# Kernel tuning notes

Hardware: AMD Instinct MI355X
Metric: run time of the kernel (lower is better)

## Reference

```python
import jax, jax.numpy as jnp
import numpy as np

B, H, W, DIM, NH, WS, SS = 32, 56, 56, 512, 16, 7, 3
L = H * W
HD = DIM // NH
N = WS * WS
SCALE = HD ** -0.5
EPS = 1e-5


def _rel_pos_index():
    coords = np.stack(np.meshgrid(np.arange(WS), np.arange(WS), indexing='ij'))  # (2,ws,ws)
    cf = coords.reshape(2, -1)
    rc = (cf[:, :, None] - cf[:, None, :]).transpose(1, 2, 0).astype(np.int64)  # (N,N,2)
    rc[..., 0] += WS - 1
    rc[..., 1] += WS - 1
    rc[..., 0] *= 2 * WS - 1
    return rc.sum(-1)  # (N,N)


def _shift_mask():
    img = np.zeros((H, W), np.float32)
    cnt = 0
    for hs in (slice(0, -WS), slice(-WS, -SS), slice(-SS, None)):
        for ws_ in (slice(0, -WS), slice(-WS, -SS), slice(-SS, None)):
            img[hs, ws_] = cnt
            cnt += 1
    m = img.reshape(H // WS, WS, W // WS, WS).transpose(0, 2, 1, 3).reshape(-1, N)  # (nW,N)
    diff = m[:, None, :] - m[:, :, None]
    return np.where(diff != 0, -100.0, 0.0).astype(np.float32)  # (nW,N,N)


REL_IDX = jnp.asarray(_rel_pos_index())
ATTN_MASK = jnp.asarray(_shift_mask())


def _ln(x, g, b):
    mu = jnp.mean(x, -1, keepdims=True)
    var = jnp.var(x, -1, keepdims=True)
    return (x - mu) * jax.lax.rsqrt(var + EPS) * g + b


def setup_inputs() -> dict:
    key = jax.random.key(0)
    ks = jax.random.split(key, 8)
    s = 0.02
    return {
        'x': jax.random.normal(ks[0], (B, L, DIM), jnp.float32),
        'norm1_g': jnp.ones((DIM,), jnp.float32),
        'norm1_b': jnp.zeros((DIM,), jnp.float32),
        'qkv_w': jax.random.normal(ks[1], (DIM, 3 * DIM), jnp.float32) * s,
        'qkv_b': jnp.zeros((3 * DIM,), jnp.float32),
        'rel_bias_table': jax.random.normal(ks[2], ((2 * WS - 1) ** 2, NH), jnp.float32) * s,
        'proj_w': jax.random.normal(ks[3], (DIM, DIM), jnp.float32) * s,
        'proj_b': jnp.zeros((DIM,), jnp.float32),
        'norm2_g': jnp.ones((DIM,), jnp.float32),
        'norm2_b': jnp.zeros((DIM,), jnp.float32),
        'fc1_w': jax.random.normal(ks[4], (DIM, 4 * DIM), jnp.float32) * s,
        'fc1_b': jnp.zeros((4 * DIM,), jnp.float32),
        'fc2_w': jax.random.normal(ks[5], (4 * DIM, DIM), jnp.float32) * s,
        'fc2_b': jnp.zeros((DIM,), jnp.float32),
    }


def reference(x, norm1_g, norm1_b, qkv_w, qkv_b, rel_bias_table, proj_w, proj_b,
              norm2_g, norm2_b, fc1_w, fc1_b, fc2_w, fc2_b):
    shortcut = x
    h = _ln(x, norm1_g, norm1_b).reshape(B, H, W, DIM)
    # cyclic shift
    h = jnp.roll(h, (-SS, -SS), axis=(1, 2))
    # window partition -> (B*nW, N, C)
    nWh, nWw = H // WS, W // WS
    h = h.reshape(B, nWh, WS, nWw, WS, DIM).transpose(0, 1, 3, 2, 4, 5).reshape(-1, N, DIM)
    Bw = h.shape[0]
    # qkv
    qkv = (h @ qkv_w + qkv_b).reshape(Bw, N, 3, NH, HD).transpose(2, 0, 3, 1, 4)
    q, k, v = qkv[0], qkv[1], qkv[2]  # (Bw, NH, N, HD)
    attn = jnp.einsum('bhnd,bhmd->bhnm', q * SCALE, k)
    # relative position bias (NH, N, N)
    bias = rel_bias_table[REL_IDX.reshape(-1)].reshape(N, N, NH).transpose(2, 0, 1)
    attn = attn + bias[None]
    # shift mask: (B, nW, NH, N, N) + (1, nW, 1, N, N)
    nW = nWh * nWw
    attn = attn.reshape(B, nW, NH, N, N) + ATTN_MASK[None, :, None]
    attn = jax.nn.softmax(attn.reshape(Bw, NH, N, N), axis=-1)
    out = jnp.einsum('bhnm,bhmd->bhnd', attn, v).transpose(0, 2, 1, 3).reshape(Bw, N, DIM)
    out = out @ proj_w + proj_b
    # window reverse + reverse shift
    out = out.reshape(B, nWh, nWw, WS, WS, DIM).transpose(0, 1, 3, 2, 4, 5).reshape(B, H, W, DIM)
    out = jnp.roll(out, (SS, SS), axis=(1, 2)).reshape(B, L, DIM)
    x = shortcut + out
    # MLP (GELU exact, matching torch nn.GELU default)
    y = _ln(x, norm2_g, norm2_b)
    y = jax.nn.gelu(y @ fc1_w + fc1_b, approximate=False) @ fc2_w + fc2_b
    return x + y
```

## Files before the change

kernel.cpp:

```cpp
#include <hip/hip_runtime.h>
#include <hip/hip_bf16.h>
#include <math.h>

#define MROWS 100352
#define MHALF 50176
#define DIM   512
#define LL    3136
#define HH    56
#define SSH   3
#define SCALE_QK 0.17677669529663687f

typedef __bf16 bf16;
typedef __bf16 bf16x8 __attribute__((ext_vector_type(8)));
typedef float  f32x4  __attribute__((ext_vector_type(4)));

typedef __attribute__((address_space(1))) void* gas_ptr;
typedef __attribute__((address_space(3))) void* las_ptr;

__device__ __forceinline__ void gload_lds16(const void* g, void* l) {
  __builtin_amdgcn_global_load_lds((gas_ptr)g, (las_ptr)l, 16, 0, 0);
}

__device__ __forceinline__ int nat_row(int r) {
  int bw = r / 49;
  int n  = r - bw * 49;
  int b  = bw >> 6;
  int wh = (bw >> 3) & 7;
  int ww = bw & 7;
  int i  = n / 7;
  int j  = n - i * 7;
  int hs = wh * 7 + i + SSH; if (hs >= HH) hs -= HH;
  int ws = ww * 7 + j + SSH; if (ws >= HH) ws -= HH;
  return b * LL + hs * HH + ws;
}

__global__ __launch_bounds__(256) void tcast_kernel(const float* __restrict__ src,
                                                    bf16* __restrict__ dst,
                                                    int Kd, int Nd) {
  __shared__ float t[32][33];
  int tx = threadIdx.x & 31, ty = threadIdx.x >> 5;
  int n0 = blockIdx.x * 32, k0 = blockIdx.y * 32;
  #pragma unroll
  for (int yy = ty; yy < 32; yy += 8)
    t[yy][tx] = src[(size_t)(k0 + yy) * Nd + n0 + tx];
  __syncthreads();
  #pragma unroll
  for (int yy = ty; yy < 32; yy += 8)
    dst[(size_t)(n0 + yy) * Kd + k0 + tx] = (bf16)t[tx][yy];
}

template<int PERM>
__global__ __launch_bounds__(256) void ln_kernel(const float* __restrict__ x,
                                                 const float* __restrict__ gw,
                                                 const float* __restrict__ bw_,
                                                 bf16* __restrict__ out) {
  int wave = threadIdx.x >> 6, lane = threadIdx.x & 63;
  int r = blockIdx.x * 4 + wave;
  int src = PERM ? nat_row(r) : r;
  const float* px = x + (size_t)src * DIM + lane * 8;
  float4 v0 = *(const float4*)px;
  float4 v1 = *(const float4*)(px + 4);
  float s = v0.x + v0.y + v0.z + v0.w + v1.x + v1.y + v1.z + v1.w;
  float q = v0.x*v0.x + v0.y*v0.y + v0.z*v0.z + v0.w*v0.w
          + v1.x*v1.x + v1.y*v1.y + v1.z*v1.z + v1.w*v1.w;
  #pragma unroll
  for (int m = 1; m < 64; m <<= 1) { s += __shfl_xor(s, m); q += __shfl_xor(q, m); }
  float mean = s * (1.f / DIM);
  float var  = q * (1.f / DIM) - mean * mean;
  float rstd = rsqrtf(var + 1e-5f);
  int c0 = lane * 8;
  float4 g0 = *(const float4*)(gw + c0),  g1 = *(const float4*)(gw + c0 + 4);
  float4 b0 = *(const float4*)(bw_ + c0), b1 = *(const float4*)(bw_ + c0 + 4);
  bf16x8 o;
  o[0] = (bf16)((v0.x - mean) * rstd * g0.x + b0.x);
  o[1] = (bf16)((v0.y - mean) * rstd * g0.y + b0.y);
  o[2] = (bf16)((v0.z - mean) * rstd * g0.z + b0.z);
  o[3] = (bf16)((v0.w - mean) * rstd * g0.w + b0.w);
  o[4] = (bf16)((v1.x - mean) * rstd * g1.x + b1.x);
  o[5] = (bf16)((v1.y - mean) * rstd * g1.y + b1.y);
  o[6] = (bf16)((v1.z - mean) * rstd * g1.z + b1.z);
  o[7] = (bf16)((v1.w - mean) * rstd * g1.w + b1.w);
  *(bf16x8*)(out + (size_t)r * DIM + c0) = o;
}


#define MF(a,b,c) __builtin_amdgcn_mfma_f32_16x16x32_bf16((a),(b),(c),0,0,0)
#define BAR() __builtin_amdgcn_s_barrier()
#define WLG() asm volatile("s_waitcnt lgkmcnt(0)" ::: "memory")
#define WVM(n) asm volatile("s_waitcnt vmcnt(" #n ")" ::: "memory")

template<int MODE, int KD, int ND>
__global__ __launch_bounds__(512, 2) void gemm256_kernel(const bf16* __restrict__ A,
                                                         const bf16* __restrict__ Bt,
                                                         const float* __restrict__ bias,
                                                         const float* __restrict__ resid,
                                                         bf16* __restrict__ outB,
                                                         float* __restrict__ outF) {
  constexpr int NTN = ND / 256;
  constexpr int NI  = KD / 128;
  __shared__ bf16 lds[65536];

  const int tid = threadIdx.x, lane = tid & 63, wv = tid >> 6;
  const int lr = lane & 15, lg = lane >> 4;
  const int wm = wv >> 2, wn = wv & 3;

  int nwg = gridDim.x, orig = blockIdx.x;
  int q = nwg >> 3, r = nwg & 7, xcd = orig & 7;
  int wgid = (xcd < r ? xcd * (q + 1) : r * (q + 1) + (xcd - r) * q) + (orig >> 3);
  int tm = wgid / NTN, tn = wgid % NTN;

  const bf16* gA = A  + (size_t)tm * 256 * KD;
  const bf16* gB = Bt + (size_t)tn * 256 * KD;

  const int klg  = (lg * 8) ^ ((lr & 8) ? 16 : 0);
  const int a_rd = (wm * 128 + lr) * 32 + klg;
  const int b_rd = (wn * 64 + lr) * 32 + klg;

  const int kbOffE = (wv >> 2) * 8192;
  const int kGlob  = (wv >> 2) * 32 + (((lane & 3) * 8) ^ ((lane & 32) ? 16 : 0));
  const int rl0    = ((wv * 2) & 7) * 16 + (lane >> 2);
  const int rl1    = rl0 + 16;
  const int c0off  = ((wv * 2) & 7) * 512;

#define STG(GP, DB, h, koff) \
  gload_lds16((GP) + (size_t)((h) * 128 + rl0) * KD + (koff) + kGlob, \
              (void*)(lds + (DB) + kbOffE + (h) * 4096 + c0off)); \
  gload_lds16((GP) + (size_t)((h) * 128 + rl1) * KD + (koff) + kGlob, \
              (void*)(lds + (DB) + kbOffE + (h) * 4096 + c0off + 512));

  f32x4 acc[8][4];
  #pragma unroll
  for (int i = 0; i < 8; i++)
    #pragma unroll
    for (int j = 0; j < 4; j++) { acc[i][j][0]=0.f; acc[i][j][1]=0.f; acc[i][j][2]=0.f; acc[i][j][3]=0.f; }

  bf16x8 Af[4][2], Bf0[2][2], Bf1[2][2];

  STG(gA, 0,     0, 0)  STG(gA, 0,     1, 0)
  STG(gB, 16384, 0, 0)  STG(gB, 16384, 1, 0)
  STG(gA, 32768, 0, 64) STG(gA, 32768, 1, 64)
  STG(gB, 49152, 0, 64) STG(gB, 49152, 1, 64)
  WVM(8); BAR();

#define PHASES(AB, BB, DOST, KST, ENDW) { \
     \
    _Pragma("unroll") for (int m = 0; m < 4; m++) { \
      Af[m][0] = *(const bf16x8*)(lds + (AB) + m * 512 + a_rd); \
      Af[m][1] = *(const bf16x8*)(lds + (AB) + 8192 + m * 512 + a_rd); } \
    _Pragma("unroll") for (int n = 0; n < 2; n++) { \
      Bf0[n][0] = *(const bf16x8*)(lds + (BB) + n * 512 + b_rd); \
      Bf0[n][1] = *(const bf16x8*)(lds + (BB) + 8192 + n * 512 + b_rd); } \
    BAR(); WLG(); __builtin_amdgcn_s_setprio(1); \
    _Pragma("unroll") for (int m = 0; m < 4; m++) \
      _Pragma("unroll") for (int n = 0; n < 2; n++) { \
        acc[m][n] = MF(Af[m][0], Bf0[n][0], acc[m][n]); \
        acc[m][n] = MF(Af[m][1], Bf0[n][1], acc[m][n]); } \
    __builtin_amdgcn_s_setprio(0); BAR(); \
     \
    _Pragma("unroll") for (int n = 0; n < 2; n++) { \
      Bf1[n][0] = *(const bf16x8*)(lds + (BB) + (n + 2) * 512 + b_rd); \
      Bf1[n][1] = *(const bf16x8*)(lds + (BB) + 8192 + (n + 2) * 512 + b_rd); } \
    if (DOST) { STG(gB, (BB), 0, (KST)) } \
    BAR(); WLG(); __builtin_amdgcn_s_setprio(1); \
    _Pragma("unroll") for (int m = 0; m < 4; m++) \
      _Pragma("unroll") for (int n = 0; n < 2; n++) { \
        acc[m][n + 2] = MF(Af[m][0], Bf1[n][0], acc[m][n + 2]); \
        acc[m][n + 2] = MF(Af[m][1], Bf1[n][1], acc[m][n + 2]); } \
    __builtin_amdgcn_s_setprio(0); BAR(); \
     \
    _Pragma("unroll") for (int m = 0; m < 4; m++) { \
      Af[m][0] = *(const bf16x8*)(lds + (AB) + (m + 4) * 512 + a_rd); \
      Af[m][1] = *(const bf16x8*)(lds + (AB) + 8192 + (m + 4) * 512 + a_rd); } \
    if (DOST) { STG(gB, (BB), 1, (KST)) STG(gA, (AB), 0, (KST)) } \
    BAR(); WLG(); __builtin_amdgcn_s_setprio(1); \
    _Pragma("unroll") for (int m = 0; m < 4; m++) \
      _Pragma("unroll") for (int n = 0; n < 2; n++) { \
        acc[m + 4][n + 2] = MF(Af[m][0], Bf1[n][0], acc[m + 4][n + 2]); \
        acc[m + 4][n + 2] = MF(Af[m][1], Bf1[n][1], acc[m + 4][n + 2]); } \
    __builtin_amdgcn_s_setprio(0); BAR(); \
     \
    if (DOST) { STG(gA, (AB), 1, (KST)) } \
    BAR(); WLG(); __builtin_amdgcn_s_setprio(1); \
    _Pragma("unroll") for (int m = 0; m < 4; m++) \
      _Pragma("unroll") for (int n = 0; n < 2; n++) { \
        acc[m + 4][n] = MF(Af[m][0], Bf0[n][0], acc[m + 4][n]); \
        acc[m + 4][n] = MF(Af[m][1], Bf0[n][1], acc[m + 4][n]); } \
    __builtin_amdgcn_s_setprio(0); ENDW; BAR(); \
  }

  #pragma unroll 1
  for (int I = 0; I < NI - 1; ++I) {
    int ke = (2 * I + 2) * 64;
    PHASES(0,     16384, 1, ke,      WVM(6));
    PHASES(32768, 49152, 1, ke + 64, WVM(6));
  }
  PHASES(0,     16384, 0, 0, WVM(0));
  PHASES(32768, 49152, 0, 0, ((void)0));

#undef PHASES
#undef STG

  #pragma unroll
  for (int fm = 0; fm < 8; fm++) {
    #pragma unroll
    for (int rr = 0; rr < 4; rr++) {
      int row = tm * 256 + wm * 128 + fm * 16 + lg * 4 + rr;
      int orow = (MODE == 1) ? nat_row(row) : row;
      #pragma unroll
      for (int fn = 0; fn < 4; fn++) {
        int col = tn * 256 + wn * 64 + fn * 16 + lr;
        float v = acc[fm][fn][rr] + bias[col];
        if (MODE == 0) {
          outB[(size_t)row * ND + col] = (bf16)v;
        } else if (MODE == 1) {
          outF[(size_t)orow * ND + col] = resid[(size_t)orow * ND + col] + v;
        } else if (MODE == 2) {
          float g = 0.5f * v * (1.f + erff(v * 0.70710678118654752f));
          outB[(size_t)row * ND + col] = (bf16)g;
        } else {
          outF[(size_t)row * ND + col] = resid[(size_t)row * ND + col] + v;
        }
      }
    }
  }
}

__global__ __launch_bounds__(256) void attn_kernel(const bf16* __restrict__ qkv,
                                                   const float* __restrict__ table,
                                                   bf16* __restrict__ attnO) {
  __shared__ bf16 P[4][64 * 72];
  int wave = threadIdx.x >> 6, lane = threadIdx.x & 63;
  int lr = lane & 15, lg = lane >> 4;
  int wid = blockIdx.x * 4 + wave;
  int win = wid >> 4, head = wid & 15;
  int wh = (win >> 3) & 7, ww = win & 7;
  const bf16* base = qkv + (size_t)win * (49 * 1536) + head * 32;

  f32x4 zero4 = {0.f, 0.f, 0.f, 0.f};
  bf16x8 aq[4], bk[4];
  #pragma unroll
  for (int mi = 0; mi < 4; mi++) {
    int qq = mi * 16 + lr; if (qq > 48) qq = 48;
    aq[mi] = *(const bf16x8*)(base + qq * 1536 + lg * 8);
    bk[mi] = *(const bf16x8*)(base + 512 + qq * 1536 + lg * 8);
  }
  f32x4 sacc[4][4];
  #pragma unroll
  for (int mi = 0; mi < 4; mi++)
    #pragma unroll
    for (int ni = 0; ni < 4; ni++)
      sacc[mi][ni] = __builtin_amdgcn_mfma_f32_16x16x32_bf16(aq[mi], bk[ni], zero4, 0, 0, 0);

  float rsum[4][4];
  #pragma unroll
  for (int mi = 0; mi < 4; mi++) {
    #pragma unroll
    for (int rr = 0; rr < 4; rr++) {
      int qrow = mi * 16 + lg * 4 + rr;
      int qc = qrow > 48 ? 48 : qrow;
      int i1 = qc / 7, j1 = qc - i1 * 7;
      int labq = ((wh < 7) ? 0 : ((i1 < 4) ? 1 : 2)) * 3 + ((ww < 7) ? 0 : ((j1 < 4) ? 1 : 2));
      float pv[4];
      float mv = -3.0e30f;
      #pragma unroll
      for (int ni = 0; ni < 4; ni++) {
        int key = ni * 16 + lr;
        float v;
        if (key > 48) {
          v = -1e30f;
        } else {
          int i2 = key / 7, j2 = key - i2 * 7;
          int labk = ((wh < 7) ? 0 : ((i2 < 4) ? 1 : 2)) * 3 + ((ww < 7) ? 0 : ((j2 < 4) ? 1 : 2));
          int idx = (i1 - i2 + 6) * 13 + (j1 - j2 + 6);
          float msk = (labq == labk) ? 0.f : -100.f;
          v = sacc[mi][ni][rr] * SCALE_QK + table[idx * 16 + head] + msk;
        }
        pv[ni] = v;
        mv = fmaxf(mv, v);
      }
      #pragma unroll
      for (int m = 1; m < 16; m <<= 1) mv = fmaxf(mv, __shfl_xor(mv, m));
      float sum = 0.f;
      #pragma unroll
      for (int ni = 0; ni < 4; ni++) {
        float p = __expf(pv[ni] - mv);
        sum += p;
        P[wave][qrow * 72 + ni * 16 + lr] = (bf16)p;
      }
      #pragma unroll
      for (int m = 1; m < 16; m <<= 1) sum += __shfl_xor(sum, m);
      rsum[mi][rr] = sum;
    }
  }
  __syncthreads();

  f32x4 oacc[4][2];
  #pragma unroll
  for (int mi = 0; mi < 4; mi++) { oacc[mi][0] = zero4; oacc[mi][1] = zero4; }
  #pragma unroll
  for (int ks = 0; ks < 2; ks++) {
    bf16x8 bv[2];
    #pragma unroll
    for (int n2 = 0; n2 < 2; n2++) {
      #pragma unroll
      for (int j = 0; j < 8; j++) {
        int kv = ks * 32 + lg * 8 + j; if (kv > 48) kv = 48;
        bv[n2][j] = base[1024 + (size_t)kv * 1536 + n2 * 16 + lr];
      }
    }
    #pragma unroll
    for (int mi = 0; mi < 4; mi++) {
      bf16x8 ap = *(const bf16x8*)(&P[wave][(mi * 16 + lr) * 72 + ks * 32 + lg * 8]);
      #pragma unroll
      for (int n2 = 0; n2 < 2; n2++)
        oacc[mi][n2] = __builtin_amdgcn_mfma_f32_16x16x32_bf16(ap, bv[n2], oacc[mi][n2], 0, 0, 0);
    }
  }
  #pragma unroll
  for (int mi = 0; mi < 4; mi++) {
    #pragma unroll
    for (int rr = 0; rr < 4; rr++) {
      int qrow = mi * 16 + lg * 4 + rr;
      if (qrow < 49) {
        float inv = 1.f / rsum[mi][rr];
        #pragma unroll
        for (int n2 = 0; n2 < 2; n2++)
          attnO[((size_t)win * 49 + qrow) * DIM + head * 32 + n2 * 16 + lr] =
              (bf16)(oacc[mi][n2][rr] * inv);
      }
    }
  }
}

extern "C" void kernel_launch(void* const* d_in, const int* in_sizes, int n_in,
                              void* d_out, int out_size, void* d_ws, size_t ws_size,
                              hipStream_t stream) {
  const float* x      = (const float*)d_in[0];
  const float* n1g    = (const float*)d_in[1];
  const float* n1b    = (const float*)d_in[2];
  const float* qkv_w  = (const float*)d_in[3];
  const float* qkv_b  = (const float*)d_in[4];
  const float* tabl   = (const float*)d_in[5];
  const float* proj_w = (const float*)d_in[6];
  const float* proj_b = (const float*)d_in[7];
  const float* n2g    = (const float*)d_in[8];
  const float* n2b    = (const float*)d_in[9];
  const float* fc1_w  = (const float*)d_in[10];
  const float* fc1_b  = (const float*)d_in[11];
  const float* fc2_w  = (const float*)d_in[12];
  const float* fc2_b  = (const float*)d_in[13];
  float* out = (float*)d_out;

  char* ws = (char*)d_ws;
  bf16*  RegA   = (bf16*)ws;
  bf16*  RegB   = (bf16*)(ws + 102760448);
  float* x2     = (float*)(ws + 102760448 + 308281344);
  bf16*  qkvWt  = (bf16*)(ws + 102760448 + 308281344 + 205520896);
  bf16*  projWt = qkvWt + 1536 * 512;
  bf16*  fc1Wt  = projWt + 512 * 512;
  bf16*  fc2Wt  = fc1Wt + 2048 * 512;

  tcast_kernel<<<dim3(1536 / 32, 512 / 32), 256, 0, stream>>>(qkv_w, qkvWt, 512, 1536);
  tcast_kernel<<<dim3(512 / 32, 512 / 32), 256, 0, stream>>>(proj_w, projWt, 512, 512);
  tcast_kernel<<<dim3(2048 / 32, 512 / 32), 256, 0, stream>>>(fc1_w, fc1Wt, 512, 2048);
  tcast_kernel<<<dim3(512 / 32, 2048 / 32), 256, 0, stream>>>(fc2_w, fc2Wt, 2048, 512);

  ln_kernel<1><<<MROWS / 4, 256, 0, stream>>>(x, n1g, n1b, RegA);
  gemm256_kernel<0, 512, 1536><<<(MROWS / 256) * 6, 512, 0, stream>>>(
      RegA, qkvWt, qkv_b, nullptr, RegB, nullptr);
  attn_kernel<<<2048 * 16 / 4, 256, 0, stream>>>(RegB, tabl, RegA);
  gemm256_kernel<1, 512, 512><<<(MROWS / 256) * 2, 512, 0, stream>>>(
      RegA, projWt, proj_b, x, nullptr, x2);
  ln_kernel<0><<<MROWS / 4, 256, 0, stream>>>(x2, n2g, n2b, RegA);
  for (int c = 0; c < 2; ++c) {
    const bf16* a1 = RegA + (size_t)c * MHALF * 512;
    gemm256_kernel<2, 512, 2048><<<(MHALF / 256) * 8, 512, 0, stream>>>(
        a1, fc1Wt, fc1_b, nullptr, RegB, nullptr);
    gemm256_kernel<3, 2048, 512><<<(MHALF / 256) * 2, 512, 0, stream>>>(
        RegB, fc2Wt, fc2_b, x2 + (size_t)c * MHALF * 512, nullptr,
        out + (size_t)c * MHALF * 512);
  }
}
```

Measured before the change: 1.704 ms.

## Write QKV in per-head attention layout and precompute bias+mask table

```diff
diff --git a/kernel.cpp b/kernel.cpp
--- a/kernel.cpp
+++ b/kernel.cpp
@@ -47,6 +47,23 @@
   #pragma unroll
   for (int yy = ty; yy < 32; yy += 8)
     dst[(size_t)(n0 + yy) * Kd + k0 + tx] = (bf16)t[tx][yy];
+}
+
+__global__ __launch_bounds__(256) void biasM_kernel(const float* __restrict__ table,
+                                                    float* __restrict__ biasM) {
+  int e = blockIdx.x * 256 + threadIdx.x;
+  if (e >= 4 * 16 * 2401) return;
+  int k  = e % 49;
+  int t  = e / 49;
+  int qv = t % 49; t /= 49;
+  int head = t & 15;
+  int cls  = t >> 4;
+  int i1 = qv / 7, j1 = qv - i1 * 7;
+  int i2 = k / 7,  j2 = k - i2 * 7;
+  float b = table[((i1 - i2 + 6) * 13 + (j1 - j2 + 6)) * 16 + head];
+  int labq = ((cls & 2) ? ((i1 < 4) ? 1 : 2) : 0) * 3 + ((cls & 1) ? ((j1 < 4) ? 1 : 2) : 0);
+  int labk = ((cls & 2) ? ((i2 < 4) ? 1 : 2) : 0) * 3 + ((cls & 1) ? ((j2 < 4) ? 1 : 2) : 0);
+  biasM[e] = b + ((labq == labk) ? 0.f : -100.f);
 }
 
 template<int PERM>
@@ -95,7 +112,9 @@
                                                          const float* __restrict__ bias,
                                                          const float* __restrict__ resid,
                                                          bf16* __restrict__ outB,
-                                                         float* __restrict__ outF) {
+                                                         float* __restrict__ outF,
+                                                         bf16* __restrict__ outK,
+                                                         bf16* __restrict__ outV) {
   constexpr int NTN = ND / 256;
   constexpr int NI  = KD / 128;
   __shared__ bf16 lds[65536];
@@ -143,7 +162,6 @@
   WVM(8); BAR();
 
 #define PHASES(AB, BB, DOST, KST, ENDW) { \
-     \
     _Pragma("unroll") for (int m = 0; m < 4; m++) { \
       Af[m][0] = *(const bf16x8*)(lds + (AB) + m * 512 + a_rd); \
       Af[m][1] = *(const bf16x8*)(lds + (AB) + 8192 + m * 512 + a_rd); } \
@@ -156,7 +174,6 @@
         acc[m][n] = MF(Af[m][0], Bf0[n][0], acc[m][n]); \
         acc[m][n] = MF(Af[m][1], Bf0[n][1], acc[m][n]); } \
     __builtin_amdgcn_s_setprio(0); BAR(); \
-     \
     _Pragma("unroll") for (int n = 0; n < 2; n++) { \
       Bf1[n][0] = *(const bf16x8*)(lds + (BB) + (n + 2) * 512 + b_rd); \
       Bf1[n][1] = *(const bf16x8*)(lds + (BB) + 8192 + (n + 2) * 512 + b_rd); } \
@@ -167,7 +184,6 @@
         acc[m][n + 2] = MF(Af[m][0], Bf1[n][0], acc[m][n + 2]); \
         acc[m][n + 2] = MF(Af[m][1], Bf1[n][1], acc[m][n + 2]); } \
     __builtin_amdgcn_s_setprio(0); BAR(); \
-     \
     _Pragma("unroll") for (int m = 0; m < 4; m++) { \
       Af[m][0] = *(const bf16x8*)(lds + (AB) + (m + 4) * 512 + a_rd); \
       Af[m][1] = *(const bf16x8*)(lds + (AB) + 8192 + (m + 4) * 512 + a_rd); } \
@@ -178,7 +194,6 @@
         acc[m + 4][n + 2] = MF(Af[m][0], Bf1[n][0], acc[m + 4][n + 2]); \
         acc[m + 4][n + 2] = MF(Af[m][1], Bf1[n][1], acc[m + 4][n + 2]); } \
     __builtin_amdgcn_s_setprio(0); BAR(); \
-     \
     if (DOST) { STG(gA, (AB), 1, (KST)) } \
     BAR(); WLG(); __builtin_amdgcn_s_setprio(1); \
     _Pragma("unroll") for (int m = 0; m < 4; m++) \
@@ -206,27 +221,36 @@
     for (int rr = 0; rr < 4; rr++) {
       int row = tm * 256 + wm * 128 + fm * 16 + lg * 4 + rr;
       int orow = (MODE == 1) ? nat_row(row) : row;
+      int win = 0, nn = 0;
+      if (MODE == 4) { win = row / 49; nn = row - win * 49; }
       #pragma unroll
       for (int fn = 0; fn < 4; fn++) {
         int col = tn * 256 + wn * 64 + fn * 16 + lr;
         float v = acc[fm][fn][rr] + bias[col];
-        if (MODE == 0) {
-          outB[(size_t)row * ND + col] = (bf16)v;
-        } else if (MODE == 1) {
+        if (MODE == 1) {
           outF[(size_t)orow * ND + col] = resid[(size_t)orow * ND + col] + v;
         } else if (MODE == 2) {
           float g = 0.5f * v * (1.f + erff(v * 0.70710678118654752f));
           outB[(size_t)row * ND + col] = (bf16)g;
-        } else {
+        } else if (MODE == 3) {
           outF[(size_t)row * ND + col] = resid[(size_t)row * ND + col] + v;
+        } else if (MODE == 4) {
+          int c = col & 511;
+          int head = c >> 5, d = c & 31;
+          size_t sb = (size_t)(win * 16 + head);
+          if (col < 512)        outB[sb * 1568 + nn * 32 + d] = (bf16)v;
+          else if (col < 1024)  outK[sb * 1568 + nn * 32 + d] = (bf16)v;
+          else                  outV[sb * 2048 + d * 64 + nn] = (bf16)v;
         }
       }
     }
   }
 }
 
-__global__ __launch_bounds__(256) void attn_kernel(const bf16* __restrict__ qkv,
-                                                   const float* __restrict__ table,
+__global__ __launch_bounds__(256) void attn_kernel(const bf16* __restrict__ Qb,
+                                                   const bf16* __restrict__ Kb,
+                                                   const bf16* __restrict__ Vt,
+                                                   const float* __restrict__ biasM,
                                                    bf16* __restrict__ attnO) {
   __shared__ bf16 P[4][64 * 72];
   int wave = threadIdx.x >> 6, lane = threadIdx.x & 63;
@@ -234,15 +258,19 @@
   int wid = blockIdx.x * 4 + wave;
   int win = wid >> 4, head = wid & 15;
   int wh = (win >> 3) & 7, ww = win & 7;
-  const bf16* base = qkv + (size_t)win * (49 * 1536) + head * 32;
+  int cls = ((wh == 7) ? 2 : 0) | ((ww == 7) ? 1 : 0);
+  const bf16* qp = Qb + (size_t)wid * 1568;
+  const bf16* kp = Kb + (size_t)wid * 1568;
+  const bf16* vp = Vt + (size_t)wid * 2048;
+  const float* bp = biasM + (size_t)cls * 38416 + head * 2401;
 
   f32x4 zero4 = {0.f, 0.f, 0.f, 0.f};
   bf16x8 aq[4], bk[4];
   #pragma unroll
   for (int mi = 0; mi < 4; mi++) {
     int qq = mi * 16 + lr; if (qq > 48) qq = 48;
-    aq[mi] = *(const bf16x8*)(base + qq * 1536 + lg * 8);
-    bk[mi] = *(const bf16x8*)(base + 512 + qq * 1536 + lg * 8);
+    aq[mi] = *(const bf16x8*)(qp + qq * 32 + lg * 8);
+    bk[mi] = *(const bf16x8*)(kp + qq * 32 + lg * 8);
   }
   f32x4 sacc[4][4];
   #pragma unroll
@@ -258,23 +286,13 @@
     for (int rr = 0; rr < 4; rr++) {
       int qrow = mi * 16 + lg * 4 + rr;
       int qc = qrow > 48 ? 48 : qrow;
-      int i1 = qc / 7, j1 = qc - i1 * 7;
-      int labq = ((wh < 7) ? 0 : ((i1 < 4) ? 1 : 2)) * 3 + ((ww < 7) ? 0 : ((j1 < 4) ? 1 : 2));
+      const float* bq = bp + qc * 49;
       float pv[4];
       float mv = -3.0e30f;
       #pragma unroll
       for (int ni = 0; ni < 4; ni++) {
         int key = ni * 16 + lr;
-        float v;
-        if (key > 48) {
-          v = -1e30f;
-        } else {
-          int i2 = key / 7, j2 = key - i2 * 7;
-          int labk = ((wh < 7) ? 0 : ((i2 < 4) ? 1 : 2)) * 3 + ((ww < 7) ? 0 : ((j2 < 4) ? 1 : 2));
-          int idx = (i1 - i2 + 6) * 13 + (j1 - j2 + 6);
-          float msk = (labq == labk) ? 0.f : -100.f;
-          v = sacc[mi][ni][rr] * SCALE_QK + table[idx * 16 + head] + msk;
-        }
+        float v = (key < 49) ? sacc[mi][ni][rr] * SCALE_QK + bq[key] : -1e30f;
         pv[ni] = v;
         mv = fmaxf(mv, v);
       }
@@ -301,13 +319,8 @@
   for (int ks = 0; ks < 2; ks++) {
     bf16x8 bv[2];
     #pragma unroll
-    for (int n2 = 0; n2 < 2; n2++) {
-      #pragma unroll
-      for (int j = 0; j < 8; j++) {
-        int kv = ks * 32 + lg * 8 + j; if (kv > 48) kv = 48;
-        bv[n2][j] = base[1024 + (size_t)kv * 1536 + n2 * 16 + lr];
-      }
-    }
+    for (int n2 = 0; n2 < 2; n2++)
+      bv[n2] = *(const bf16x8*)(vp + (n2 * 16 + lr) * 64 + ks * 32 + lg * 8);
     #pragma unroll
     for (int mi = 0; mi < 4; mi++) {
       bf16x8 ap = *(const bf16x8*)(&P[wave][(mi * 16 + lr) * 72 + ks * 32 + lg * 8]);
@@ -353,31 +366,37 @@
 
   char* ws = (char*)d_ws;
   bf16*  RegA   = (bf16*)ws;
-  bf16*  RegB   = (bf16*)(ws + 102760448);
-  float* x2     = (float*)(ws + 102760448 + 308281344);
-  bf16*  qkvWt  = (bf16*)(ws + 102760448 + 308281344 + 205520896);
+  bf16*  Qb     = (bf16*)(ws + 102760448);
+  bf16*  Kb     = (bf16*)(ws + 102760448 + 102760448);
+  bf16*  RegB   = Qb;
+  char*  reg2   = ws + 411041792;
+  bf16*  Vt     = (bf16*)reg2;
+  float* biasM  = (float*)(reg2 + 134217728);
+  float* x2     = (float*)reg2;
+  bf16*  qkvWt  = (bf16*)(ws + 616562688);
   bf16*  projWt = qkvWt + 1536 * 512;
   bf16*  fc1Wt  = projWt + 512 * 512;
   bf16*  fc2Wt  = fc1Wt + 2048 * 512;
 
+  biasM_kernel<<<(4 * 16 * 2401 + 255) / 256, 256, 0, stream>>>(tabl, biasM);
   tcast_kernel<<<dim3(1536 / 32, 512 / 32), 256, 0, stream>>>(qkv_w, qkvWt, 512, 1536);
   tcast_kernel<<<dim3(512 / 32, 512 / 32), 256, 0, stream>>>(proj_w, projWt, 512, 512);
   tcast_kernel<<<dim3(2048 / 32, 512 / 32), 256, 0, stream>>>(fc1_w, fc1Wt, 512, 2048);
   tcast_kernel<<<dim3(512 / 32, 2048 / 32), 256, 0, stream>>>(fc2_w, fc2Wt, 2048, 512);
 
   ln_kernel<1><<<MROWS / 4, 256, 0, stream>>>(x, n1g, n1b, RegA);
-  gemm256_kernel<0, 512, 1536><<<(MROWS / 256) * 6, 512, 0, stream>>>(
-      RegA, qkvWt, qkv_b, nullptr, RegB, nullptr);
-  attn_kernel<<<2048 * 16 / 4, 256, 0, stream>>>(RegB, tabl, RegA);
+  gemm256_kernel<4, 512, 1536><<<(MROWS / 256) * 6, 512, 0, stream>>>(
+      RegA, qkvWt, qkv_b, nullptr, Qb, nullptr, Kb, Vt);
+  attn_kernel<<<2048 * 16 / 4, 256, 0, stream>>>(Qb, Kb, Vt, biasM, RegA);
   gemm256_kernel<1, 512, 512><<<(MROWS / 256) * 2, 512, 0, stream>>>(
-      RegA, projWt, proj_b, x, nullptr, x2);
+      RegA, projWt, proj_b, x, nullptr, x2, nullptr, nullptr);
   ln_kernel<0><<<MROWS / 4, 256, 0, stream>>>(x2, n2g, n2b, RegA);
   for (int c = 0; c < 2; ++c) {
     const bf16* a1 = RegA + (size_t)c * MHALF * 512;
     gemm256_kernel<2, 512, 2048><<<(MHALF / 256) * 8, 512, 0, stream>>>(
-        a1, fc1Wt, fc1_b, nullptr, RegB, nullptr);
+        a1, fc1Wt, fc1_b, nullptr, RegB, nullptr, nullptr, nullptr);
     gemm256_kernel<3, 2048, 512><<<(MHALF / 256) * 2, 512, 0, stream>>>(
         RegB, fc2Wt, fc2_b, x2 + (size_t)c * MHALF * 512, nullptr,
-        out + (size_t)c * MHALF * 512);
-  }
-}
+        out + (size_t)c * MHALF * 512, nullptr, nullptr);
+  }
+}
```

Measured after the change: 1.755 ms. 1.03x slower.
